# Kernel tuning notes

Measured on AMD Instinct MI355X. Metric: run time of the kernel, lower is better.

Reference implementation:

```python
import jax, jax.numpy as jnp
import numpy as np

N = 8192
IN_F = 512
OUT_F = 64
ALPHA = 0.2  # LeakyReLU negative slope
NEG_INF = -9e15


def setup_inputs() -> dict:
    key = jax.random.key(0)
    k1, k2, k3, k4 = jax.random.split(key, 4)
    x = jax.random.normal(k1, (N, IN_F), dtype=jnp.float32)
    adj = jax.random.randint(k2, (N, N), 0, 2, dtype=jnp.int32)
    # xavier_uniform with gain=1.414
    def xavier(k, shape, gain=1.414):
        fan_in, fan_out = shape[0], shape[1]
        a = gain * np.sqrt(6.0 / (fan_in + fan_out))
        return jax.random.uniform(k, shape, jnp.float32, -a, a)
    W = xavier(k3, (IN_F, OUT_F))
    a = xavier(k4, (2 * OUT_F, 1))
    return {"x": x, "adj": adj, "W": W, "a": a}


def reference(x, adj, W, a):
    h = x @ W  # [N, F]
    f = W.shape[1]
    # e[i,j] = leakyrelu([h_i, h_j] @ a) = leakyrelu(h_i@a1 + h_j@a2)
    e1 = h @ a[:f, 0]   # [N]
    e2 = h @ a[f:, 0]   # [N]
    e = jax.nn.leaky_relu(e1[:, None] + e2[None, :], negative_slope=ALPHA)  # [N, N]
    scores = jnp.where(adj > 0, e, NEG_INF)
    attention = jax.nn.softmax(scores, axis=1)  # dropout p=0.0 -> identity
    h_prime = attention @ h  # [N, F]
    return jax.nn.elu(h_prime)  # concat=True
```

## Files before the change

kernel.cpp:

```cpp
#include <hip/hip_runtime.h>
#include <hip/hip_bf16.h>

#define NN 8192
#define KF 512
#define FF 64
#define GAT_ALPHA 0.2f
#define MSHIFT 20.0f
#define LOG2E 1.44269504f

#define JSPLIT 16
#define JW (NN / JSPLIT)
#define KSTEPS (JW / 32)

#define HTS 520

#define EXP2F(x) __builtin_amdgcn_exp2f(x)

typedef __attribute__((ext_vector_type(8))) __bf16 bf16x8;
typedef __attribute__((ext_vector_type(4))) float f32x4;

__device__ __forceinline__ unsigned pack_bf16_rne(float hi, float lo) {
    unsigned uh = __float_as_uint(hi);
    unsigned ul = __float_as_uint(lo);
    uh = uh + 0x7FFFu + ((uh >> 16) & 1u);
    ul = ul + 0x7FFFu + ((ul >> 16) & 1u);
    return (uh & 0xFFFF0000u) | (ul >> 16);
}

__global__ __launch_bounds__(256) void gat_linear(
    const float* __restrict__ x, const float* __restrict__ W,
    const float* __restrict__ av, __hip_bfloat16* __restrict__ ht,
    float* __restrict__ e1, float* __restrict__ e2)
{
    __shared__ float xs[32][33];
    __shared__ float Ws[32][64];
    __shared__ float ep[2][32][17];

    const int t  = threadIdx.x;
    const int fq = t & 15;
    const int rq = t >> 4;
    const int i0 = blockIdx.x * 32;

    const int kl = t & 31, r0 = t >> 5;
    const int fw = t & 63, kq = t >> 6;

    float acc[2][4] = {};

    for (int kt = 0; kt < KF; kt += 32) {
        #pragma unroll
        for (int m = 0; m < 4; ++m)
            xs[kl][r0 + 8 * m] = x[(size_t)(i0 + r0 + 8 * m) * KF + kt + kl];
        #pragma unroll
        for (int m = 0; m < 8; ++m)
            Ws[kq + 4 * m][fw] = W[(size_t)(kt + kq + 4 * m) * FF + fw];
        __syncthreads();
        #pragma unroll
        for (int kk = 0; kk < 32; ++kk) {
            float x0 = xs[kk][rq * 2];
            float x1 = xs[kk][rq * 2 + 1];
            f32x4 wv = *(const f32x4*)&Ws[kk][fq * 4];
            #pragma unroll
            for (int v = 0; v < 4; ++v) {
                acc[0][v] += x0 * wv[v];
                acc[1][v] += x1 * wv[v];
            }
        }
        __syncthreads();
    }

    #pragma unroll
    for (int v = 0; v < 4; ++v) {
        int f = fq * 4 + v;
        unsigned w = pack_bf16_rne(acc[1][v], acc[0][v]);
        *(unsigned*)&ht[(size_t)f * NN + i0 + rq * 2] = w;
    }

    f32x4 a1v = *(const f32x4*)&av[fq * 4];
    f32x4 a2v = *(const f32x4*)&av[64 + fq * 4];
    #pragma unroll
    for (int u = 0; u < 2; ++u) {
        float s1 = 0.f, s2 = 0.f;
        #pragma unroll
        for (int v = 0; v < 4; ++v) {
            s1 += acc[u][v] * a1v[v];
            s2 += acc[u][v] * a2v[v];
        }
        ep[0][rq * 2 + u][fq] = s1;
        ep[1][rq * 2 + u][fq] = s2;
    }
    __syncthreads();
    if (t < 32) {
        float s1 = 0.f, s2 = 0.f;
        #pragma unroll
        for (int q = 0; q < 16; ++q) { s1 += ep[0][t][q]; s2 += ep[1][t][q]; }
        e1[i0 + t] = s1 * LOG2E;
        e2[i0 + t] = s2 * LOG2E;
    }
}

__global__ __launch_bounds__(256) void gat_attn(
    const int* __restrict__ adj, const __hip_bfloat16* __restrict__ ht,
    const float* __restrict__ e1, const float* __restrict__ e2,
    float* __restrict__ accs, float* __restrict__ lsums)
{
    __shared__ __hip_bfloat16 hs[64 * HTS];
    __shared__ float e2s[JW];
    __shared__ unsigned char msk[KSTEPS * 4 * 68];

    const int t     = threadIdx.x;
    const int lane  = t & 63;
    const int wv    = t >> 6;
    const int n16   = lane & 15;
    const int quad  = lane >> 4;
    const int split = blockIdx.x & (JSPLIT - 1);
    const int i0b   = (blockIdx.x >> 4) * 64;
    const int i0    = i0b + wv * 16;
    const int j0    = split * JW;
    const int rowl  = wv * 16 + n16;
    const int row   = i0 + n16;

    #pragma unroll
    for (int k = 0; k < 16; ++k) {
        int g  = t + k * 256;
        int f  = g >> 6;
        int jl = (g & 63) * 8;
        *(bf16x8*)&hs[f * HTS + jl] =
            *(const bf16x8*)&ht[(size_t)f * NN + j0 + jl];
    }
    if (t < JW / 4)
        *(float4*)&e2s[t * 4] = *(const float4*)&e2[j0 + t * 4];

    {
        const int st = t & 15;
        #pragma unroll
        for (int rep = 0; rep < 4; ++rep) {
            const int r = rep * 16 + (t >> 4);
            const int* ap = adj + (size_t)(i0b + r) * NN + j0 + st * 32;
            unsigned w = 0;
            #pragma unroll
            for (int k = 0; k < 8; ++k) {
                int4 v = *(const int4*)(ap + k * 4);
                unsigned nib =  (unsigned)(v.x > 0)
                             | ((unsigned)(v.y > 0) << 1)
                             | ((unsigned)(v.z > 0) << 2)
                             | ((unsigned)(v.w > 0) << 3);
                w |= nib << (k * 4);
            }
            msk[(st * 4 + 0) * 68 + r] = (unsigned char)(w       & 0xFF);
            msk[(st * 4 + 1) * 68 + r] = (unsigned char)((w >> 8)  & 0xFF);
            msk[(st * 4 + 2) * 68 + r] = (unsigned char)((w >> 16) & 0xFF);
            msk[(st * 4 + 3) * 68 + r] = (unsigned char)((w >> 24) & 0xFF);
        }
    }
    __syncthreads();

    const float e1L = e1[row];
    float ms = e1L + MSHIFT * LOG2E;
    const float miL = ms > 0.f ? ms : GAT_ALPHA * ms;
    const float c0  = e1L - miL;
    const float c1  = GAT_ALPHA * e1L - miL;

    const __hip_bfloat16* hp = hs + rowl * 0 + n16 * HTS + quad * 8;
    const float* ep0 = e2s + quad * 8;

    f32x4 dacc0 = {0.f,0.f,0.f,0.f}, dacc1 = {0.f,0.f,0.f,0.f};
    f32x4 dacc2 = {0.f,0.f,0.f,0.f}, dacc3 = {0.f,0.f,0.f,0.f};
    f32x4 dl    = {0.f,0.f,0.f,0.f};

    typedef __attribute__((ext_vector_type(4))) int i32x4;
    const i32x4 ones_i = {0x3F803F80, 0x3F803F80, 0x3F803F80, 0x3F803F80};
    const bf16x8 ones  = __builtin_bit_cast(bf16x8, ones_i);

    unsigned mb = msk[(0 * 4 + quad) * 68 + rowl];
    f32x4  e0 = *(const f32x4*)(ep0);
    f32x4  ev = *(const f32x4*)(ep0 + 4);
    bf16x8 b0 = *(const bf16x8*)(hp);
    bf16x8 b1 = *(const bf16x8*)(hp + 16 * HTS);
    bf16x8 b2 = *(const bf16x8*)(hp + 32 * HTS);
    bf16x8 b3 = *(const bf16x8*)(hp + 48 * HTS);

    for (int st = 0; st < KSTEPS; ++st) {
        const unsigned mc = mb;
        const f32x4  ce0 = e0, cev = ev;
        const bf16x8 cb0 = b0, cb1 = b1, cb2 = b2, cb3 = b3;
        if (st + 1 < KSTEPS) {
            mb = msk[((st + 1) * 4 + quad) * 68 + rowl];
            e0 = *(const f32x4*)(ep0 + (st + 1) * 32);
            ev = *(const f32x4*)(ep0 + (st + 1) * 32 + 4);
            b0 = *(const bf16x8*)(hp + (st + 1) * 32);
            b1 = *(const bf16x8*)(hp + 16 * HTS + (st + 1) * 32);
            b2 = *(const bf16x8*)(hp + 32 * HTS + (st + 1) * 32);
            b3 = *(const bf16x8*)(hp + 48 * HTS + (st + 1) * 32);
        }

#define PJ(eval, bit)                                                          \
        ( ((mc >> (bit)) & 1u)                                                 \
            ? EXP2F(fmaxf(c0 + (eval), __builtin_fmaf(GAT_ALPHA, (eval), c1))) \
            : 0.f )
        float p0 = PJ(ce0.x, 0);
        float p1 = PJ(ce0.y, 1);
        float p2 = PJ(ce0.z, 2);
        float p3 = PJ(ce0.w, 3);
        float p4 = PJ(cev.x, 4);
        float p5 = PJ(cev.y, 5);
        float p6 = PJ(cev.z, 6);
        float p7 = PJ(cev.w, 7);
#undef PJ
        i32x4 iv;
        iv.x = (int)pack_bf16_rne(p1, p0);
        iv.y = (int)pack_bf16_rne(p3, p2);
        iv.z = (int)pack_bf16_rne(p5, p4);
        iv.w = (int)pack_bf16_rne(p7, p6);
        bf16x8 af = __builtin_bit_cast(bf16x8, iv);

        dacc0 = __builtin_amdgcn_mfma_f32_16x16x32_bf16(af, cb0, dacc0, 0, 0, 0);
        dacc1 = __builtin_amdgcn_mfma_f32_16x16x32_bf16(af, cb1, dacc1, 0, 0, 0);
        dacc2 = __builtin_amdgcn_mfma_f32_16x16x32_bf16(af, cb2, dacc2, 0, 0, 0);
        dacc3 = __builtin_amdgcn_mfma_f32_16x16x32_bf16(af, cb3, dacc3, 0, 0, 0);
        dl    = __builtin_amdgcn_mfma_f32_16x16x32_bf16(af, ones, dl, 0, 0, 0);
    }

    if (n16 == 0) {
        lsums[(size_t)split * NN + i0 + quad * 4 + 0] = dl.x;
        lsums[(size_t)split * NN + i0 + quad * 4 + 1] = dl.y;
        lsums[(size_t)split * NN + i0 + quad * 4 + 2] = dl.z;
        lsums[(size_t)split * NN + i0 + quad * 4 + 3] = dl.w;
    }

    float* ab = accs + (size_t)split * NN * FF + (size_t)(i0 + quad * 4) * FF + n16;
#define STORE4(dv, ftofs)                                                      \
    ab[0 * FF + (ftofs)] = (dv).x;                                             \
    ab[1 * FF + (ftofs)] = (dv).y;                                             \
    ab[2 * FF + (ftofs)] = (dv).z;                                             \
    ab[3 * FF + (ftofs)] = (dv).w;
    STORE4(dacc0, 0)
    STORE4(dacc1, 16)
    STORE4(dacc2, 32)
    STORE4(dacc3, 48)
#undef STORE4
}

__global__ __launch_bounds__(256) void gat_epilogue(
    const float* __restrict__ accs, const float* __restrict__ lsums,
    float* __restrict__ out)
{
    const int idx = (blockIdx.x * 256 + threadIdx.x) * 4;
    const int row = idx >> 6;

    float l = 0.f;
    #pragma unroll
    for (int s = 0; s < JSPLIT; ++s) l += lsums[(size_t)s * NN + row];

    f32x4 a = {0.f, 0.f, 0.f, 0.f};
    #pragma unroll
    for (int s = 0; s < JSPLIT; ++s) {
        f32x4 v = *(const f32x4*)(accs + (size_t)s * NN * FF + idx);
        a.x += v.x; a.y += v.y; a.z += v.z; a.w += v.w;
    }

    const float li = 1.f / l;
    f32x4 o;
    o.x = a.x * li; o.y = a.y * li; o.z = a.z * li; o.w = a.w * li;
    o.x = o.x > 0.f ? o.x : __expf(o.x) - 1.f;
    o.y = o.y > 0.f ? o.y : __expf(o.y) - 1.f;
    o.z = o.z > 0.f ? o.z : __expf(o.z) - 1.f;
    o.w = o.w > 0.f ? o.w : __expf(o.w) - 1.f;
    *(f32x4*)(out + idx) = o;
}

extern "C" void kernel_launch(void* const* d_in, const int* in_sizes, int n_in,
                              void* d_out, int out_size, void* d_ws, size_t ws_size,
                              hipStream_t stream) {
    const float* x   = (const float*)d_in[0];
    const int*   adj = (const int*)d_in[1];
    const float* W   = (const float*)d_in[2];
    const float* av  = (const float*)d_in[3];
    float* out = (float*)d_out;

    char* wsb = (char*)d_ws;
    __hip_bfloat16* ht = (__hip_bfloat16*)wsb;
    float* e1    = (float*)(wsb + (1 << 20));
    float* e2    = e1 + NN;
    float* accs  = e2 + NN;
    float* lsums = accs + (size_t)JSPLIT * NN * FF;

    gat_linear<<<256, 256, 0, stream>>>(x, W, av, ht, e1, e2);
    gat_attn<<<(NN / 64) * JSPLIT, 256, 0, stream>>>(adj, ht, e1, e2, accs, lsums);
    gat_epilogue<<<NN * FF / 1024, 256, 0, stream>>>(accs, lsums, out);
}
```

Measured before the change: 399.8 us.

## Halve j-splits and double-buffer h tiles through registers in attention kernel

Cuts the number of column splits from 16 to 8, so each block covers 1024 columns. The h tile is streamed in four 256-column sub-tiles, double-buffered in LDS, and the next sub-tile's global loads are issued into registers before the current MFMA work. The adjacency mask is now stored as packed 32-bit words per row. This halves the partial accumulator and lsum writes, and the reduction traffic that follows them, and hides the h load latency. In exchange it adds per-sub-tile barriers, uses more registers for the prefetch, and launches half as many blocks.

```diff
diff --git a/kernel.cpp b/kernel.cpp
--- a/kernel.cpp
+++ b/kernel.cpp
@@ -8,16 +8,18 @@
 #define MSHIFT 20.0f
 #define LOG2E 1.44269504f
 
-#define JSPLIT 16
+#define JSPLIT 8
 #define JW (NN / JSPLIT)
-#define KSTEPS (JW / 32)
-
-#define HTS 520
+#define NSUB 4
+#define SUBJ 256
+#define SUBK 8
+#define HTS 264
 
 #define EXP2F(x) __builtin_amdgcn_exp2f(x)
 
 typedef __attribute__((ext_vector_type(8))) __bf16 bf16x8;
 typedef __attribute__((ext_vector_type(4))) float f32x4;
+typedef __attribute__((ext_vector_type(4))) int   i32x4;
 
 __device__ __forceinline__ unsigned pack_bf16_rne(float hi, float lo) {
     unsigned uh = __float_as_uint(hi);
@@ -103,9 +105,9 @@
     const float* __restrict__ e1, const float* __restrict__ e2,
     float* __restrict__ accs, float* __restrict__ lsums)
 {
-    __shared__ __hip_bfloat16 hs[64 * HTS];
+    __shared__ __hip_bfloat16 hs[2][64 * HTS];
+    __shared__ unsigned msk32[64 * 33];
     __shared__ float e2s[JW];
-    __shared__ unsigned char msk[KSTEPS * 4 * 68];
 
     const int t     = threadIdx.x;
     const int lane  = t & 63;
@@ -113,29 +115,19 @@
     const int n16   = lane & 15;
     const int quad  = lane >> 4;
     const int split = blockIdx.x & (JSPLIT - 1);
-    const int i0b   = (blockIdx.x >> 4) * 64;
+    const int i0b   = (blockIdx.x >> 3) * 64;
     const int i0    = i0b + wv * 16;
     const int j0    = split * JW;
     const int rowl  = wv * 16 + n16;
     const int row   = i0 + n16;
 
-    #pragma unroll
-    for (int k = 0; k < 16; ++k) {
-        int g  = t + k * 256;
-        int f  = g >> 6;
-        int jl = (g & 63) * 8;
-        *(bf16x8*)&hs[f * HTS + jl] =
-            *(const bf16x8*)&ht[(size_t)f * NN + j0 + jl];
-    }
-    if (t < JW / 4)
-        *(float4*)&e2s[t * 4] = *(const float4*)&e2[j0 + t * 4];
-
     {
-        const int st = t & 15;
-        #pragma unroll
-        for (int rep = 0; rep < 4; ++rep) {
-            const int r = rep * 16 + (t >> 4);
-            const int* ap = adj + (size_t)(i0b + r) * NN + j0 + st * 32;
+        const int stt = t & 31;
+        const int rr  = t >> 5;
+        #pragma unroll
+        for (int rep = 0; rep < 8; ++rep) {
+            const int r = rep * 8 + rr;
+            const int* ap = adj + (size_t)(i0b + r) * NN + j0 + stt * 32;
             unsigned w = 0;
             #pragma unroll
             for (int k = 0; k < 8; ++k) {
@@ -146,11 +138,14 @@
                              | ((unsigned)(v.w > 0) << 3);
                 w |= nib << (k * 4);
             }
-            msk[(st * 4 + 0) * 68 + r] = (unsigned char)(w       & 0xFF);
-            msk[(st * 4 + 1) * 68 + r] = (unsigned char)((w >> 8)  & 0xFF);
-            msk[(st * 4 + 2) * 68 + r] = (unsigned char)((w >> 16) & 0xFF);
-            msk[(st * 4 + 3) * 68 + r] = (unsigned char)((w >> 24) & 0xFF);
-        }
+            msk32[r * 33 + stt] = w;
+        }
+    }
+    *(float4*)&e2s[t * 4] = *(const float4*)&e2[j0 + t * 4];
+    #pragma unroll
+    for (int c = 0; c < 8; ++c) {
+        int g = t + c * 256, f = g >> 5, jl = (g & 31) * 8;
+        *(bf16x8*)&hs[0][f * HTS + jl] = *(const bf16x8*)&ht[(size_t)f * NN + j0 + jl];
     }
     __syncthreads();
 
@@ -160,64 +155,75 @@
     const float c0  = e1L - miL;
     const float c1  = GAT_ALPHA * e1L - miL;
 
-    const __hip_bfloat16* hp = hs + rowl * 0 + n16 * HTS + quad * 8;
     const float* ep0 = e2s + quad * 8;
 
     f32x4 dacc0 = {0.f,0.f,0.f,0.f}, dacc1 = {0.f,0.f,0.f,0.f};
     f32x4 dacc2 = {0.f,0.f,0.f,0.f}, dacc3 = {0.f,0.f,0.f,0.f};
     f32x4 dl    = {0.f,0.f,0.f,0.f};
 
-    typedef __attribute__((ext_vector_type(4))) int i32x4;
     const i32x4 ones_i = {0x3F803F80, 0x3F803F80, 0x3F803F80, 0x3F803F80};
     const bf16x8 ones  = __builtin_bit_cast(bf16x8, ones_i);
 
-    unsigned mb = msk[(0 * 4 + quad) * 68 + rowl];
-    f32x4  e0 = *(const f32x4*)(ep0);
-    f32x4  ev = *(const f32x4*)(ep0 + 4);
-    bf16x8 b0 = *(const bf16x8*)(hp);
-    bf16x8 b1 = *(const bf16x8*)(hp + 16 * HTS);
-    bf16x8 b2 = *(const bf16x8*)(hp + 32 * HTS);
-    bf16x8 b3 = *(const bf16x8*)(hp + 48 * HTS);
-
-    for (int st = 0; st < KSTEPS; ++st) {
-        const unsigned mc = mb;
-        const f32x4  ce0 = e0, cev = ev;
-        const bf16x8 cb0 = b0, cb1 = b1, cb2 = b2, cb3 = b3;
-        if (st + 1 < KSTEPS) {
-            mb = msk[((st + 1) * 4 + quad) * 68 + rowl];
-            e0 = *(const f32x4*)(ep0 + (st + 1) * 32);
-            ev = *(const f32x4*)(ep0 + (st + 1) * 32 + 4);
-            b0 = *(const bf16x8*)(hp + (st + 1) * 32);
-            b1 = *(const bf16x8*)(hp + 16 * HTS + (st + 1) * 32);
-            b2 = *(const bf16x8*)(hp + 32 * HTS + (st + 1) * 32);
-            b3 = *(const bf16x8*)(hp + 48 * HTS + (st + 1) * 32);
-        }
+    for (int sub = 0; sub < NSUB; ++sub) {
+        const int buf = sub & 1;
+
+        bf16x8 hreg[8];
+        if (sub + 1 < NSUB) {
+            #pragma unroll
+            for (int c = 0; c < 8; ++c) {
+                int g = t + c * 256, f = g >> 5, jl = (g & 31) * 8;
+                hreg[c] = *(const bf16x8*)&ht[(size_t)f * NN + j0 + (sub + 1) * SUBJ + jl];
+            }
+        }
+
+        #pragma unroll
+        for (int k = 0; k < SUBK; ++k) {
+            const int stg = sub * SUBK + k;
+            unsigned mw = msk32[rowl * 33 + stg];
+            unsigned mc = mw >> (quad * 8);
+            f32x4 e0 = *(const f32x4*)(ep0 + stg * 32);
+            f32x4 ev = *(const f32x4*)(ep0 + stg * 32 + 4);
+            const __hip_bfloat16* hb = &hs[buf][n16 * HTS + k * 32 + quad * 8];
+            bf16x8 b0 = *(const bf16x8*)(hb);
+            bf16x8 b1 = *(const bf16x8*)(hb + 16 * HTS);
+            bf16x8 b2 = *(const bf16x8*)(hb + 32 * HTS);
+            bf16x8 b3 = *(const bf16x8*)(hb + 48 * HTS);
 
 #define PJ(eval, bit)                                                          \
-        ( ((mc >> (bit)) & 1u)                                                 \
-            ? EXP2F(fmaxf(c0 + (eval), __builtin_fmaf(GAT_ALPHA, (eval), c1))) \
-            : 0.f )
-        float p0 = PJ(ce0.x, 0);
-        float p1 = PJ(ce0.y, 1);
-        float p2 = PJ(ce0.z, 2);
-        float p3 = PJ(ce0.w, 3);
-        float p4 = PJ(cev.x, 4);
-        float p5 = PJ(cev.y, 5);
-        float p6 = PJ(cev.z, 6);
-        float p7 = PJ(cev.w, 7);
+            ( ((mc >> (bit)) & 1u)                                             \
+                ? EXP2F(fmaxf(c0 + (eval), __builtin_fmaf(GAT_ALPHA, (eval), c1))) \
+                : 0.f )
+            float p0 = PJ(e0.x, 0);
+            float p1 = PJ(e0.y, 1);
+            float p2 = PJ(e0.z, 2);
+            float p3 = PJ(e0.w, 3);
+            float p4 = PJ(ev.x, 4);
+            float p5 = PJ(ev.y, 5);
+            float p6 = PJ(ev.z, 6);
+            float p7 = PJ(ev.w, 7);
 #undef PJ
-        i32x4 iv;
-        iv.x = (int)pack_bf16_rne(p1, p0);
-        iv.y = (int)pack_bf16_rne(p3, p2);
-        iv.z = (int)pack_bf16_rne(p5, p4);
-        iv.w = (int)pack_bf16_rne(p7, p6);
-        bf16x8 af = __builtin_bit_cast(bf16x8, iv);
-
-        dacc0 = __builtin_amdgcn_mfma_f32_16x16x32_bf16(af, cb0, dacc0, 0, 0, 0);
-        dacc1 = __builtin_amdgcn_mfma_f32_16x16x32_bf16(af, cb1, dacc1, 0, 0, 0);
-        dacc2 = __builtin_amdgcn_mfma_f32_16x16x32_bf16(af, cb2, dacc2, 0, 0, 0);
-        dacc3 = __builtin_amdgcn_mfma_f32_16x16x32_bf16(af, cb3, dacc3, 0, 0, 0);
-        dl    = __builtin_amdgcn_mfma_f32_16x16x32_bf16(af, ones, dl, 0, 0, 0);
+            i32x4 iv;
+            iv.x = (int)pack_bf16_rne(p1, p0);
+            iv.y = (int)pack_bf16_rne(p3, p2);
+            iv.z = (int)pack_bf16_rne(p5, p4);
+            iv.w = (int)pack_bf16_rne(p7, p6);
+            bf16x8 af = __builtin_bit_cast(bf16x8, iv);
+
+            dacc0 = __builtin_amdgcn_mfma_f32_16x16x32_bf16(af, b0, dacc0, 0, 0, 0);
+            dacc1 = __builtin_amdgcn_mfma_f32_16x16x32_bf16(af, b1, dacc1, 0, 0, 0);
+            dacc2 = __builtin_amdgcn_mfma_f32_16x16x32_bf16(af, b2, dacc2, 0, 0, 0);
+            dacc3 = __builtin_amdgcn_mfma_f32_16x16x32_bf16(af, b3, dacc3, 0, 0, 0);
+            dl    = __builtin_amdgcn_mfma_f32_16x16x32_bf16(af, ones, dl, 0, 0, 0);
+        }
+
+        if (sub + 1 < NSUB) {
+            #pragma unroll
+            for (int c = 0; c < 8; ++c) {
+                int g = t + c * 256, f = g >> 5, jl = (g & 31) * 8;
+                *(bf16x8*)&hs[buf ^ 1][f * HTS + jl] = hreg[c];
+            }
+        }
+        __syncthreads();
     }
 
     if (n16 == 0) {
```

Result: slower. 416.3 us (+4.1%).
